# Optimization experiments

Measured on AMD Instinct MI355X. Metric: run time of the kernel, lower is better.

Reference implementation:

```python
import jax, jax.numpy as jnp
import numpy as np

D = 2  # NUM_DIM (spatial dimension)


def _mlp(x, params, activate_final=False):
    n = len(params)
    for i, (w, b) in enumerate(params):
        x = x @ w + b
        if i < n - 1 or activate_final:
            x = jnp.tanh(x)
    return x


def _glorot(key, shape):
    fan_in, fan_out = shape[0], shape[-1]
    lim = np.sqrt(6.0 / (fan_in + fan_out)).astype(np.float32)
    return jax.random.uniform(key, shape, jnp.float32, -lim, lim)


def setup_inputs() -> dict:
    key = jax.random.key(0)
    ks = iter(jax.random.split(key, 40))
    B, N, M, K, P, C = 4, 32, 64, 16, 128, 2
    AW, TW, W = 64, 256, 128
    inp = {}
    inp['phase_coords'] = jax.random.normal(next(ks), (B, N, 2 * D), jnp.float32)
    inp['boundary_coords'] = jax.random.normal(next(ks), (B, M, 2 * D), jnp.float32)
    inp['boundary'] = jax.random.uniform(next(ks), (B, M), jnp.float32)
    inp['boundary_weights'] = jax.random.uniform(next(ks), (B, M), jnp.float32)
    inp['position_coords'] = jax.random.normal(next(ks), (B, P, D), jnp.float32)
    inp['sigma'] = jax.random.uniform(next(ks), (B, P, C), jnp.float32)
    inp['velocity_coords'] = jax.random.normal(next(ks), (B, K, D), jnp.float32)
    inp['velocity_weights'] = jax.random.uniform(next(ks), (B, K), jnp.float32)
    inp['scattering_kernel'] = jax.random.uniform(next(ks), (B, N, K), jnp.float32)
    inp['self_scattering_kernel'] = jax.random.uniform(next(ks), (B, K, K), jnp.float32)
    # attention MLP: input 2*D + 2 (coords ++ local frame) -> [64, 64, 1]
    inp['aw0'] = _glorot(next(ks), (2 * D + 2, AW)); inp['ab0'] = jnp.zeros((AW,), jnp.float32)
    inp['aw1'] = _glorot(next(ks), (AW, AW)); inp['ab1'] = jnp.zeros((AW,), jnp.float32)
    inp['aw2'] = _glorot(next(ks), (AW, 1)); inp['ab2'] = jnp.zeros((1,), jnp.float32)
    # transport MLP: input 4*D + C -> [256, 256, 128], activate_final=True
    inp['tw0'] = _glorot(next(ks), (4 * D + C, TW)); inp['tb0'] = jnp.zeros((TW,), jnp.float32)
    inp['tw1'] = _glorot(next(ks), (TW, TW)); inp['tb1'] = jnp.zeros((TW,), jnp.float32)
    inp['tw2'] = _glorot(next(ks), (TW, W)); inp['tb2'] = jnp.zeros((W,), jnp.float32)
    # scattering modules: res_block_depth=2 -> one stacked layer + one final layer
    inp['sw0'] = _glorot(next(ks), (W, W))
    inp['sb0'] = jax.random.uniform(next(ks), (W,), jnp.float32, -0.1, 0.1)
    inp['sw1'] = _glorot(next(ks), (W, W))
    inp['sb1'] = jax.random.uniform(next(ks), (W,), jnp.float32, -0.1, 0.1)
    inp['out_w'] = jax.random.uniform(next(ks), (W,), jnp.float32, -0.1, 0.1)
    return inp


def _forward(phase_coords, boundary_coords, boundary, boundary_weights,
             position_coords, sigma, velocity_coords, velocity_weights,
             scattering_kernel, self_scattering_kernel,
             aw0, ab0, aw1, ab1, aw2, ab2,
             tw0, tb0, tw1, tb1, tw2, tb2,
             sw0, sb0, sw1, sb1, out_w):
    B, N, _ = phase_coords.shape
    M = boundary_coords.shape[1]
    K = velocity_coords.shape[1]
    P = position_coords.shape[1]
    C = sigma.shape[-1]
    K1 = K + 1  # phase velocity v plus the Nv quadrature velocities

    x, v = phase_coords[..., :D], phase_coords[..., D:]          # (B,N,D)
    xp, vp = boundary_coords[..., :D], boundary_coords[..., D:]  # (B,M,D)

    # all velocities at which the transport MLP is evaluated: (B,N,K1,D)
    vall = jnp.concatenate(
        [v[:, :, None, :],
         jnp.broadcast_to(velocity_coords[:, None, :, :], (B, N, K, D))], axis=2)

    # ---- CoefficientNet (geometry-masked MLP attention over coeff positions) ----
    coords = jnp.concatenate(
        [jnp.broadcast_to(x[:, :, None, :], (B, N, K1, D)), vall], axis=-1)  # (B,N,K1,2D)
    ang_g = vall / jnp.sqrt(jnp.sum(vall ** 2, axis=-1, keepdims=True) + 1e-16)
    rel = x[:, :, None, :] - position_coords[:, None, :, :]                 # (B,N,P,D)
    rel_dist = jnp.sqrt(jnp.sum(rel ** 2, axis=-1) + 1e-16)                 # (B,N,P)
    pos_local = jnp.einsum('bnpd,bnkd->bnkp', rel, ang_g)                   # (B,N,K1,P)
    ang_local = pos_local / (rel_dist[:, :, None, :] + 1e-8)
    frames = jnp.stack([ang_local, pos_local], axis=-1)                     # (B,N,K1,P,2)
    qk = jnp.concatenate(
        [jnp.broadcast_to(coords[:, :, :, None, :], (B, N, K1, P, 2 * D)), frames], axis=-1)
    logits = _mlp(qk, [(aw0, ab0), (aw1, ab1), (aw2, ab2)])[..., 0]         # (B,N,K1,P)
    attn_w = jax.nn.softmax(jnp.where(pos_local > 0, logits, -1e30), axis=-1)
    coeff = jnp.exp(-jnp.einsum('bnkp,bpc->bnkc', attn_w, sigma))           # (B,N,K1,C)

    # ---- TransportModule: MLP + exp over (B,N,M,K1) ----
    t_in = jnp.concatenate([
        jnp.broadcast_to(x[:, :, None, None, :], (B, N, M, K1, D)),
        jnp.broadcast_to(vall[:, :, None, :, :], (B, N, M, K1, D)),
        jnp.broadcast_to(xp[:, None, :, None, :], (B, N, M, K1, D)),
        jnp.broadcast_to(vp[:, None, :, None, :], (B, N, M, K1, D)),
        jnp.broadcast_to(coeff[:, :, None, :, :], (B, N, M, K1, C)),
    ], axis=-1)
    g = jnp.exp(_mlp(t_in, [(tw0, tb0), (tw1, tb1), (tw2, tb2)], activate_final=True))
    act_v = g[:, :, :, 0, :]       # (B,N,M,W)  at the phase velocity
    act_vstar = g[:, :, :, 1:, :]  # (B,N,M,K,W) at the quadrature velocities

    rw_v = (1.0 - scattering_kernel) * velocity_weights[:, None, :]        # (B,N,K)
    rw_vs = (1.0 - self_scattering_kernel) * velocity_weights[:, None, :]  # (B,K,K)

    def scat_v(act, sw, sb):
        res = jnp.einsum('bnk,bnmkw->bnmw', rw_v, act)
        return jnp.tanh(jnp.einsum('iw,bnmw->bnmi', sw, res) + sb)

    def scat_vs(act, sw, sb):
        res = jnp.einsum('bij,bnmjw->bnmiw', rw_vs, act)
        return jnp.tanh(jnp.einsum('iw,bnmkw->bnmki', sw, res) + sb)

    # layer_stack block (res_block_depth - 1 = 1 layer, shared params within the layer)
    new_v = act_v + scat_v(act_vstar, sw0, sb0)
    act_vstar = act_vstar + scat_vs(act_vstar, sw0, sb0)
    act_v = new_v
    # final scattering module (fresh params) updating act_v with res_weights_v
    green = act_v + scat_v(act_vstar, sw1, sb1)

    gdot = jnp.einsum('bnmw,w->bnm', green, out_w)
    # quadrature over boundary points
    return jnp.einsum('bnm,bm->bn', gdot, boundary * boundary_weights)


def reference(phase_coords, boundary_coords, boundary, boundary_weights,
              position_coords, sigma, velocity_coords, velocity_weights,
              scattering_kernel, self_scattering_kernel,
              aw0, ab0, aw1, ab1, aw2, ab2,
              tw0, tb0, tw1, tb1, tw2, tb2,
              sw0, sb0, sw1, sb1, out_w):
    return _forward(phase_coords, boundary_coords, boundary, boundary_weights,
                    position_coords, sigma, velocity_coords, velocity_weights,
                    scattering_kernel, self_scattering_kernel,
                    aw0, ab0, aw1, ab1, aw2, ab2,
                    tw0, tb0, tw1, tb1, tw2, tb2,
                    sw0, sb0, sw1, sb1, out_w)
```

## Files before the change

### kernel.cpp

```cpp
#include <hip/hip_runtime.h>
#include <hip/hip_bf16.h>

#define BB 4
#define NN 32
#define MM 64
#define KK 16
#define KK1 17
#define PP 128
#define CC 2

typedef unsigned short ushort_t;
typedef unsigned int uint32;
typedef __attribute__((ext_vector_type(8))) short bhalf8;
typedef __attribute__((ext_vector_type(4))) float floatx4;

#define TK  2.885390082f
#define L2E 1.44269504f

__device__ __forceinline__ float tanh_pre(float xs) {
    float e = __builtin_amdgcn_exp2f(xs);
    return fmaf(-2.0f, __builtin_amdgcn_rcpf(e + 1.0f), 1.0f);
}

__device__ __forceinline__ ushort_t f2b(float f) {
    uint32 u = __float_as_uint(f);
    return (ushort_t)((u + 0x8000u) >> 16);
}
__device__ __forceinline__ float b2f(ushort_t h) {
    return __uint_as_float(((uint32)h) << 16);
}

__device__ __forceinline__ bhalf8 tanh_uw(bhalf8 u, bhalf8 w) {
    bhalf8 h;
    #pragma unroll
    for (int j = 0; j < 8; ++j)
        h[j] = (short)f2b(tanh_pre(b2f((ushort_t)u[j]) + b2f((ushort_t)w[j])));
    return h;
}

__global__ void prep_kernel(const float* __restrict__ tw0, const float* __restrict__ tw1,
                            const float* __restrict__ tw2, const float* __restrict__ sw0,
                            const float* __restrict__ sw1, const float* __restrict__ aw0,
                            const float* __restrict__ aw1, const float* __restrict__ tb0,
                            const float* __restrict__ bcoord,
                            ushort_t* __restrict__ W1t, ushort_t* __restrict__ W2t,
                            ushort_t* __restrict__ S0t, ushort_t* __restrict__ S1t,
                            ushort_t* __restrict__ W0a, ushort_t* __restrict__ W1a,
                            ushort_t* __restrict__ w_ws) {
    int i = blockIdx.x * 256 + threadIdx.x;
    if (i < 65536) {
        int nn = i >> 8, k = i & 255;
        W1t[i] = f2b(tw1[k * 256 + nn]);
    } else if (i < 98304) {
        int j = i - 65536; int nn = j >> 8, k = j & 255;
        W2t[j] = f2b(tw2[k * 128 + nn]);
    } else if (i < 114688) {
        S0t[i - 98304] = f2b(sw0[i - 98304]);
    } else if (i < 131072) {
        S1t[i - 114688] = f2b(sw1[i - 114688]);
    } else if (i < 133120) {
        int j = i - 131072; int nn = j >> 5, k = j & 31;
        W0a[j] = (k < 6) ? f2b(aw0[k * 64 + nn]) : (ushort_t)0;
    } else if (i < 137216) {
        int j = i - 133120; int nn = j >> 6, k = j & 63;
        W1a[j] = f2b(aw1[k * 64 + nn]);
    } else if (i < 202752) {
        int j = i - 137216;
        int m = j >> 8, c = j & 255;
        float v = bcoord[m * 4 + 0] * tw0[4 * 256 + c]
                + bcoord[m * 4 + 1] * tw0[5 * 256 + c]
                + bcoord[m * 4 + 2] * tw0[6 * 256 + c]
                + bcoord[m * 4 + 3] * tw0[7 * 256 + c]
                + tb0[c];
        w_ws[j] = f2b(v * TK);
    }
}

#define AH0S 72

__global__ __launch_bounds__(128, 4) void attn_kernel(
    const float* __restrict__ phase, const float* __restrict__ posc,
    const float* __restrict__ sigma, const float* __restrict__ velc,
    const ushort_t* __restrict__ W0a, const ushort_t* __restrict__ W1a,
    const float* __restrict__ ab0, const float* __restrict__ ab1,
    const float* __restrict__ aw2, const float* __restrict__ ab2,
    const float* __restrict__ tw0, ushort_t* __restrict__ u_ws)
{
    __shared__ __align__(16) ushort_t sAH[128 * AH0S];
    __shared__ float sPL[128];
    __shared__ float sLG[128];
    __shared__ float s_red[8];

    const int tid = threadIdx.x;
    const int wave = tid >> 6;
    const int lane = tid & 63;
    const int lrow = lane & 15;
    const int lkg  = lane >> 4;

    const int blk = blockIdx.x;
    const int b = blk / (NN * KK1);
    const int rem = blk % (NN * KK1);
    const int n = rem / KK1;
    const int k = rem % KK1;

    float x0, x1, va0, va1;
    {
        const int p = tid;
        x0 = phase[(b * NN + n) * 4 + 0];
        x1 = phase[(b * NN + n) * 4 + 1];
        if (k == 0) { va0 = phase[(b * NN + n) * 4 + 2]; va1 = phase[(b * NN + n) * 4 + 3]; }
        else { va0 = velc[(b * KK + (k - 1)) * 2 + 0]; va1 = velc[(b * KK + (k - 1)) * 2 + 1]; }
        const float inv = rsqrtf(va0 * va0 + va1 * va1 + 1e-16f);
        const float ag0 = va0 * inv, ag1 = va1 * inv;
        const float px = posc[(b * PP + p) * 2 + 0];
        const float py = posc[(b * PP + p) * 2 + 1];
        const float r0 = x0 - px, r1 = x1 - py;
        const float rd = sqrtf(r0 * r0 + r1 * r1 + 1e-16f);
        const float pl = r0 * ag0 + r1 * ag1;
        const float al = pl * __builtin_amdgcn_rcpf(rd + 1e-8f);
        sPL[p] = pl;
        bhalf8 f0;
        f0[0] = (short)f2b(x0); f0[1] = (short)f2b(x1);
        f0[2] = (short)f2b(va0); f0[3] = (short)f2b(va1);
        f0[4] = (short)f2b(al); f0[5] = (short)f2b(pl);
        f0[6] = 0; f0[7] = 0;
        bhalf8 z = {0, 0, 0, 0, 0, 0, 0, 0};
        *(bhalf8*)&sAH[p * 32 + 0] = f0;
        *(bhalf8*)&sAH[p * 32 + 8] = z;
        *(bhalf8*)&sAH[p * 32 + 16] = z;
        *(bhalf8*)&sAH[p * 32 + 24] = z;
    }
    __syncthreads();

    {
        float b0v[4];
        #pragma unroll
        for (int j = 0; j < 4; ++j) b0v[j] = ab0[j * 16 + lrow] * TK;
        bhalf8 a[4];
        #pragma unroll
        for (int mtl = 0; mtl < 4; ++mtl)
            a[mtl] = *(const bhalf8*)&sAH[(wave * 64 + mtl * 16 + lrow) * 32 + lkg * 8];
        __syncthreads();
        #pragma unroll
        for (int j = 0; j < 4; ++j) {
            bhalf8 bf = *(const bhalf8*)(W0a + (j * 16 + lrow) * 32 + lkg * 8);
            #pragma unroll
            for (int mtl = 0; mtl < 4; ++mtl) {
                floatx4 c = {0.f, 0.f, 0.f, 0.f};
                c = __builtin_amdgcn_mfma_f32_16x16x32_bf16(a[mtl], bf, c, 0, 0, 0);
                #pragma unroll
                for (int q = 0; q < 4; ++q) {
                    int row = wave * 64 + mtl * 16 + lkg * 4 + q;
                    sAH[row * AH0S + j * 16 + lrow] = f2b(tanh_pre(fmaf(c[q], TK, b0v[j])));
                }
            }
        }
    }
    __syncthreads();

    {
        float b1v[4], w2v[4];
        #pragma unroll
        for (int j = 0; j < 4; ++j) { b1v[j] = ab1[j * 16 + lrow] * TK; w2v[j] = aw2[j * 16 + lrow]; }
        bhalf8 a0[4], a1[4];
        #pragma unroll
        for (int mtl = 0; mtl < 4; ++mtl) {
            int base = (wave * 64 + mtl * 16 + lrow) * AH0S;
            a0[mtl] = *(const bhalf8*)&sAH[base + lkg * 8];
            a1[mtl] = *(const bhalf8*)&sAH[base + 32 + lkg * 8];
        }
        float s[4][4];
        #pragma unroll
        for (int mtl = 0; mtl < 4; ++mtl)
            #pragma unroll
            for (int q = 0; q < 4; ++q) s[mtl][q] = 0.0f;
        #pragma unroll
        for (int j = 0; j < 4; ++j) {
            bhalf8 bf0 = *(const bhalf8*)(W1a + (j * 16 + lrow) * 64 + lkg * 8);
            bhalf8 bf1 = *(const bhalf8*)(W1a + (j * 16 + lrow) * 64 + 32 + lkg * 8);
            #pragma unroll
            for (int mtl = 0; mtl < 4; ++mtl) {
                floatx4 c = {0.f, 0.f, 0.f, 0.f};
                c = __builtin_amdgcn_mfma_f32_16x16x32_bf16(a0[mtl], bf0, c, 0, 0, 0);
                c = __builtin_amdgcn_mfma_f32_16x16x32_bf16(a1[mtl], bf1, c, 0, 0, 0);
                #pragma unroll
                for (int q = 0; q < 4; ++q)
                    s[mtl][q] += tanh_pre(fmaf(c[q], TK, b1v[j])) * w2v[j];
            }
        }
        #pragma unroll
        for (int mask = 1; mask <= 8; mask <<= 1)
            #pragma unroll
            for (int mtl = 0; mtl < 4; ++mtl)
                #pragma unroll
                for (int q = 0; q < 4; ++q)
                    s[mtl][q] += __shfl_xor(s[mtl][q], mask, 64);
        if (lrow == 0) {
            #pragma unroll
            for (int mtl = 0; mtl < 4; ++mtl)
                #pragma unroll
                for (int q = 0; q < 4; ++q)
                    sLG[wave * 64 + mtl * 16 + lkg * 4 + q] = s[mtl][q];
        }
    }
    __syncthreads();

    {
        const int p = tid;
        const float ml = (sPL[p] > 0.0f) ? (sLG[p] + ab2[0]) : -1e30f;
        const int wid = wave;
        float mv = ml;
        for (int o = 32; o > 0; o >>= 1) mv = fmaxf(mv, __shfl_xor(mv, o, 64));
        if (lane == 0) s_red[wid] = mv;
        __syncthreads();
        mv = fmaxf(s_red[0], s_red[1]);

        const float ew = __expf(ml - mv);
        float sv = ew;
        for (int o = 32; o > 0; o >>= 1) sv += __shfl_xor(sv, o, 64);
        if (lane == 0) s_red[2 + wid] = sv;
        __syncthreads();
        sv = s_red[2] + s_red[3];
        const float attn = ew * __builtin_amdgcn_rcpf(sv);

        float s0 = attn * sigma[(b * PP + p) * 2 + 0];
        float s1 = attn * sigma[(b * PP + p) * 2 + 1];
        for (int o = 32; o > 0; o >>= 1) { s0 += __shfl_xor(s0, o, 64); s1 += __shfl_xor(s1, o, 64); }
        if (lane == 0) { s_red[4 + wid] = s0; s_red[6 + wid] = s1; }
        __syncthreads();

        const float cc0 = __expf(-(s_red[4] + s_red[5]));
        const float cc1 = __expf(-(s_red[6] + s_red[7]));
        const float x0k = x0 * TK, x1k = x1 * TK;
        const float va0k = va0 * TK, va1k = va1 * TK;
        const float cc0k = cc0 * TK, cc1k = cc1 * TK;
        const int ubase = ((b * NN + n) * KK1 + k) * 256;
        for (int cc = tid; cc < 256; cc += 128) {
            float uv = x0k * tw0[cc] + x1k * tw0[256 + cc]
                     + va0k * tw0[512 + cc] + va1k * tw0[768 + cc]
                     + cc0k * tw0[2048 + cc] + cc1k * tw0[2304 + cc];
            u_ws[ubase + cc] = f2b(uv);
        }
    }
}

#define H0S  264
#define H1S  136
#define GTSs 40
#define AS2S 136

#define U_H0A  0
#define U_GTS  0
#define U_A2S  5128
#define U_H1A  8976
#define U_AS2  8976
#define U_A3   8976
#define U_AS   13600
#define F_BBW  7072
#define F_RED  7074

__global__ __launch_bounds__(256, 4) void transport_kernel(
    const float* __restrict__ boundary, const float* __restrict__ bweights,
    const float* __restrict__ vweights, const float* __restrict__ scat,
    const float* __restrict__ selfscat,
    const ushort_t* __restrict__ W1t, const ushort_t* __restrict__ W2t,
    const ushort_t* __restrict__ S0t, const ushort_t* __restrict__ S1t,
    const float* __restrict__ tb1, const float* __restrict__ tb2,
    const float* __restrict__ sb0, const float* __restrict__ sb1,
    const float* __restrict__ outw,
    const ushort_t* __restrict__ u_ws, const ushort_t* __restrict__ w_ws,
    float* __restrict__ out)
{
    __shared__ __align__(16) ushort_t smem[14160];
    float* smf = (float*)smem;

    const int tid = threadIdx.x;
    const int wave = tid >> 6;
    const int lane = tid & 63;
    const int lrow = lane & 15;
    const int lkg  = lane >> 4;

    const int blk = blockIdx.x;
    const int b  = blk >> 10;
    const int n  = (blk >> 5) & 31;
    const int mg = blk & 31;
    const int m0 = mg * 2;
    const int bn = b * NN + n;

    if (tid < 2)
        smf[F_BBW + tid] = boundary[b * MM + m0 + tid] * bweights[b * MM + m0 + tid];

    for (int idx = tid; idx < 17 * 32; idx += 256) {
        int i = idx >> 5, c = idx & 31;
        float val = 0.0f;
        if (c < 16) {
            float vw = vweights[b * KK + c];
            val = (i < 16) ? (1.0f - selfscat[(b * KK + i) * KK + c]) * vw
                           : (1.0f - scat[bn * KK + c]) * vw;
        }
        smem[U_AS + idx] = f2b(val);
    }

    {
        const int r0  = tid >> 5;
        const int oct = tid & 31;
        const int co  = oct * 8;
        const int rC  = 16 + r0;
        const int mlC = (rC >= 17) ? 1 : 0;
        const int kC  = rC - 17 * mlC;
        const bhalf8 wml0 = *(const bhalf8*)(w_ws + (b * MM + m0 + 0) * 256 + co);
        const bhalf8 wml1 = *(const bhalf8*)(w_ws + (b * MM + m0 + 1) * 256 + co);
        const bhalf8 uA = *(const bhalf8*)(u_ws + (bn * KK1 + r0) * 256 + co);
        const bhalf8 uB = *(const bhalf8*)(u_ws + (bn * KK1 + 8 + r0) * 256 + co);
        const bhalf8 uC = *(const bhalf8*)(u_ws + (bn * KK1 + kC) * 256 + co);
        const bhalf8 uD = *(const bhalf8*)(u_ws + (bn * KK1 + 7 + r0) * 256 + co);
        bhalf8 uE;
        if (r0 < 2)
            uE = *(const bhalf8*)(u_ws + (bn * KK1 + 15 + r0) * 256 + co);
        *(bhalf8*)&smem[U_H0A + r0 * H0S + co]        = tanh_uw(uA, wml0);
        *(bhalf8*)&smem[U_H0A + (8 + r0) * H0S + co]  = tanh_uw(uB, wml0);
        *(bhalf8*)&smem[U_H0A + rC * H0S + co]        = tanh_uw(uC, mlC ? wml1 : wml0);
        *(bhalf8*)&smem[U_H0A + (24 + r0) * H0S + co] = tanh_uw(uD, wml1);
        if (r0 < 2)
            *(bhalf8*)&smem[U_H0A + (32 + r0) * H0S + co] = tanh_uw(uE, wml1);
    }
    __syncthreads();

    floatx4 c2[2][3];
    #pragma unroll
    for (int j = 0; j < 2; ++j)
        #pragma unroll
        for (int mt = 0; mt < 3; ++mt) c2[j][mt] = (floatx4){0.f, 0.f, 0.f, 0.f};

    #pragma unroll
    for (int p = 0; p < 2; ++p) {
        floatx4 c1h[2][3];
        #pragma unroll
        for (int j = 0; j < 2; ++j)
            #pragma unroll
            for (int mt = 0; mt < 3; ++mt) c1h[j][mt] = (floatx4){0.f, 0.f, 0.f, 0.f};
        #pragma unroll
        for (int ksl = 0; ksl < 8; ++ksl) {
            bhalf8 a[3];
            #pragma unroll
            for (int mt = 0; mt < 3; ++mt)
                a[mt] = *(const bhalf8*)&smem[U_H0A + (mt * 16 + lrow) * H0S + ksl * 32 + lkg * 8];
            #pragma unroll
            for (int jj = 0; jj < 2; ++jj) {
                bhalf8 bf = *(const bhalf8*)(W1t + ((4 * wave + 2 * p + jj) * 16 + lrow) * 256
                                             + ksl * 32 + lkg * 8);
                #pragma unroll
                for (int mt = 0; mt < 3; ++mt)
                    c1h[jj][mt] = __builtin_amdgcn_mfma_f32_16x16x32_bf16(a[mt], bf, c1h[jj][mt], 0, 0, 0);
            }
        }
        #pragma unroll
        for (int jj = 0; jj < 2; ++jj) {
            const float bb = tb1[(4 * wave + 2 * p + jj) * 16 + lrow] * TK;
            #pragma unroll
            for (int mt = 0; mt < 3; ++mt)
                #pragma unroll
                for (int q = 0; q < 4; ++q) {
                    const int row = mt * 16 + lkg * 4 + q;
                    if (row < 34)
                        smem[U_H1A + row * H1S + wave * 32 + jj * 16 + lrow] =
                            f2b(tanh_pre(fmaf(c1h[jj][mt][q], TK, bb)));
                }
        }
        __syncthreads();
        if (p == 1) {
            bhalf8 z = {0, 0, 0, 0, 0, 0, 0, 0};
            if (tid < 128)       *(bhalf8*)&smem[U_GTS + tid * GTSs + 32] = z;
            else if (tid == 128) *(bhalf8*)&smem[U_GTS + 5120] = z;
        }
        #pragma unroll
        for (int ks = 0; ks < 4; ++ks) {
            bhalf8 a[3];
            #pragma unroll
            for (int mt = 0; mt < 3; ++mt) {
                int rr = mt * 16 + lrow;
                if (rr >= 34) rr = 32;
                a[mt] = *(const bhalf8*)&smem[U_H1A + rr * H1S + ks * 32 + lkg * 8];
            }
            #pragma unroll
            for (int j2 = 0; j2 < 2; ++j2) {
                bhalf8 bf = *(const bhalf8*)(W2t + ((2 * wave + j2) * 16 + lrow) * 256
                                             + ks * 64 + p * 32 + lkg * 8);
                #pragma unroll
                for (int mt = 0; mt < 3; ++mt)
                    c2[j2][mt] = __builtin_amdgcn_mfma_f32_16x16x32_bf16(a[mt], bf, c2[j2][mt], 0, 0, 0);
            }
        }
        if (p == 0) __syncthreads();
    }

    float gv0[2] = {0.f, 0.f}, gv1[2] = {0.f, 0.f};
    {
        #pragma unroll
        for (int j = 0; j < 2; ++j) {
            const float bb = tb2[(2 * wave + j) * 16 + lrow] * TK;
            #pragma unroll
            for (int mt = 0; mt < 3; ++mt)
                #pragma unroll
                for (int q = 0; q < 4; ++q) {
                    int row = mt * 16 + lkg * 4 + q;
                    if (row < 34) {
                        int ml = (row >= 17);
                        int k = row - ml * 17;
                        int col = (2 * wave + j) * 16 + lrow;
                        float t = tanh_pre(fmaf(c2[j][mt][q], TK, bb));
                        float g = __builtin_amdgcn_exp2f(t * L2E);
                        if (k == 0) { if (ml) gv1[j] = g; else gv0[j] = g; }
                        else        smem[U_GTS + col * GTSs + ml * 16 + (k - 1)] = f2b(g);
                    }
                }
        }
    }
    __syncthreads();

    for (int idx = tid; idx < 512; idx += 256) {
        int r = idx >> 5, c = idx & 31;
        smem[U_A2S + idx] = ((c >> 4) == r) ? smem[U_AS + 16 * 32 + (c & 15)] : (ushort_t)0;
    }
    {
        bhalf8 a0 = *(const bhalf8*)&smem[U_AS + lrow * 32 + lkg * 8];
        bhalf8 a1 = *(const bhalf8*)&smem[U_AS + 16 * 32 + lkg * 8];
        for (int m = 0; m < 2; ++m) {
            #pragma unroll
            for (int j = 0; j < 2; ++j) {
                int nt = 2 * wave + j;
                bhalf8 bf = *(const bhalf8*)&smem[U_GTS + (nt * 16 + lrow) * GTSs + m * 16 + lkg * 8];
                #pragma unroll
                for (int mt = 0; mt < 2; ++mt) {
                    floatx4 c = {0.f, 0.f, 0.f, 0.f};
                    c = __builtin_amdgcn_mfma_f32_16x16x32_bf16(mt ? a1 : a0, bf, c, 0, 0, 0);
                    #pragma unroll
                    for (int q = 0; q < 4; ++q) {
                        int ic = mt * 16 + lkg * 4 + q;
                        if (ic < 17) {
                            int r2 = (ic == 16) ? m * 17 : m * 17 + 1 + ic;
                            smem[U_AS2 + r2 * AS2S + nt * 16 + lrow] = f2b(c[q]);
                        }
                    }
                }
            }
        }
    }
    __syncthreads();

    float nv0[2] = {0.f, 0.f}, nv1[2] = {0.f, 0.f};
    {
        floatx4 c3[2][3];
        #pragma unroll
        for (int j = 0; j < 2; ++j)
            #pragma unroll
            for (int mt = 0; mt < 3; ++mt) c3[j][mt] = (floatx4){0.f, 0.f, 0.f, 0.f};
        #pragma unroll
        for (int ks = 0; ks < 4; ++ks) {
            bhalf8 a[3];
            #pragma unroll
            for (int mt = 0; mt < 3; ++mt) {
                int rr = mt * 16 + lrow;
                if (rr >= 34) rr = 32;
                a[mt] = *(const bhalf8*)&smem[U_AS2 + rr * AS2S + ks * 32 + lkg * 8];
            }
            #pragma unroll
            for (int j = 0; j < 2; ++j) {
                bhalf8 bf = *(const bhalf8*)(S0t + ((2 * wave + j) * 16 + lrow) * 128 + ks * 32 + lkg * 8);
                #pragma unroll
                for (int mt = 0; mt < 3; ++mt)
                    c3[j][mt] = __builtin_amdgcn_mfma_f32_16x16x32_bf16(a[mt], bf, c3[j][mt], 0, 0, 0);
            }
        }
        #pragma unroll
        for (int j = 0; j < 2; ++j) {
            const float bb = sb0[(2 * wave + j) * 16 + lrow] * TK;
            #pragma unroll
            for (int mt = 0; mt < 3; ++mt)
                #pragma unroll
                for (int q = 0; q < 4; ++q) {
                    int r2 = mt * 16 + lkg * 4 + q;
                    if (r2 < 34) {
                        int m = (r2 >= 17);
                        int i2 = r2 - m * 17;
                        int col = (2 * wave + j) * 16 + lrow;
                        float val = tanh_pre(fmaf(c3[j][mt][q], TK, bb));
                        if (i2 == 0) {
                            if (m) nv1[j] = gv1[j] + val; else nv0[j] = gv0[j] + val;
                        } else {
                            int cell = U_GTS + col * GTSs + m * 16 + (i2 - 1);
                            smem[cell] = f2b(b2f(smem[cell]) + val);
                        }
                    }
                }
        }
    }
    __syncthreads();

    {
        bhalf8 a = *(const bhalf8*)&smem[U_A2S + lrow * 32 + lkg * 8];
        #pragma unroll
        for (int j = 0; j < 2; ++j) {
            int nt = 2 * wave + j;
            bhalf8 bf = *(const bhalf8*)&smem[U_GTS + (nt * 16 + lrow) * GTSs + lkg * 8];
            floatx4 c = {0.f, 0.f, 0.f, 0.f};
            c = __builtin_amdgcn_mfma_f32_16x16x32_bf16(a, bf, c, 0, 0, 0);
            #pragma unroll
            for (int q = 0; q < 4; ++q) {
                int r = lkg * 4 + q;
                smem[U_A3 + r * AS2S + nt * 16 + lrow] = f2b(c[q]);
            }
        }
    }
    __syncthreads();

    float acc = 0.0f;
    {
        bhalf8 a[4];
        #pragma unroll
        for (int ks = 0; ks < 4; ++ks)
            a[ks] = *(const bhalf8*)&smem[U_A3 + lrow * AS2S + ks * 32 + lkg * 8];
        #pragma unroll
        for (int j = 0; j < 2; ++j) {
            int nt = 2 * wave + j;
            float s1v = sb1[nt * 16 + lrow] * TK;
            float owv = outw[nt * 16 + lrow];
            floatx4 c = {0.f, 0.f, 0.f, 0.f};
            #pragma unroll
            for (int ks = 0; ks < 4; ++ks) {
                bhalf8 bf = *(const bhalf8*)(S1t + (nt * 16 + lrow) * 128 + ks * 32 + lkg * 8);
                c = __builtin_amdgcn_mfma_f32_16x16x32_bf16(a[ks], bf, c, 0, 0, 0);
            }
            if (lkg == 0) {
                #pragma unroll
                for (int q = 0; q < 2; ++q) {
                    float green = (q ? nv1[j] : nv0[j]) + tanh_pre(fmaf(c[q], TK, s1v));
                    acc += green * owv * smf[F_BBW + q];
                }
            }
        }
    }
    for (int o = 32; o > 0; o >>= 1) acc += __shfl_xor(acc, o, 64);
    if (lane == 0) smf[F_RED + wave] = acc;
    __syncthreads();
    if (tid == 0) {
        float tot = smf[F_RED + 0] + smf[F_RED + 1] + smf[F_RED + 2] + smf[F_RED + 3];
        atomicAdd(&out[bn], tot);
    }
}

extern "C" void kernel_launch(void* const* d_in, const int* in_sizes, int n_in,
                              void* d_out, int out_size, void* d_ws, size_t ws_size,
                              hipStream_t stream) {
    const float* phase    = (const float*)d_in[0];
    const float* bcoord   = (const float*)d_in[1];
    const float* boundary = (const float*)d_in[2];
    const float* bweights = (const float*)d_in[3];
    const float* posc     = (const float*)d_in[4];
    const float* sigma    = (const float*)d_in[5];
    const float* velc     = (const float*)d_in[6];
    const float* vweights = (const float*)d_in[7];
    const float* scat     = (const float*)d_in[8];
    const float* selfscat = (const float*)d_in[9];
    const float* aw0 = (const float*)d_in[10];
    const float* ab0 = (const float*)d_in[11];
    const float* aw1 = (const float*)d_in[12];
    const float* ab1 = (const float*)d_in[13];
    const float* aw2 = (const float*)d_in[14];
    const float* ab2 = (const float*)d_in[15];
    const float* tw0 = (const float*)d_in[16];
    const float* tb0 = (const float*)d_in[17];
    const float* tw1 = (const float*)d_in[18];
    const float* tb1 = (const float*)d_in[19];
    const float* tw2 = (const float*)d_in[20];
    const float* tb2 = (const float*)d_in[21];
    const float* sw0 = (const float*)d_in[22];
    const float* sb0 = (const float*)d_in[23];
    const float* sw1 = (const float*)d_in[24];
    const float* sb1 = (const float*)d_in[25];
    const float* outw = (const float*)d_in[26];

    float* out = (float*)d_out;
    char* ws = (char*)d_ws;
    ushort_t* W1t  = (ushort_t*)(ws + 0);
    ushort_t* W2t  = (ushort_t*)(ws + 131072);
    ushort_t* S0t  = (ushort_t*)(ws + 196608);
    ushort_t* S1t  = (ushort_t*)(ws + 229376);
    ushort_t* W0a  = (ushort_t*)(ws + 262144);
    ushort_t* W1a  = (ushort_t*)(ws + 266240);
    ushort_t* u_ws = (ushort_t*)(ws + 274432);
    ushort_t* w_ws = (ushort_t*)(ws + 1388544);

    hipMemsetAsync(d_out, 0, (size_t)out_size * sizeof(float), stream);

    prep_kernel<<<792, 256, 0, stream>>>(tw0, tw1, tw2, sw0, sw1, aw0, aw1, tb0, bcoord,
                                         W1t, W2t, S0t, S1t, W0a, W1a, w_ws);

    attn_kernel<<<BB * NN * KK1, 128, 0, stream>>>(
        phase, posc, sigma, velc, W0a, W1a, ab0, ab1, aw2, ab2, tw0, u_ws);

    transport_kernel<<<BB * NN * 32, 256, 0, stream>>>(
        boundary, bweights, vweights, scat, selfscat,
        W1t, W2t, S0t, S1t, tb1, tb2, sb0, sb1, outw, u_ws, w_ws, out);
}
```

Measured before the change: 261.9 us.

## Widen attention kernel to 256 threads and merge softmax reductions

The attention kernel now launches 256 threads per block instead of 128, so each of the four waves handles 32 positions in the MLP MFMA stages instead of 64. The softmax sum and the sigma-weighted sums are reduced in one pass, with normalization applied afterwards, which removes one block barrier. The final projection writes one output per thread. The aim is more parallelism and less per-wave serial work in this small kernel, at the cost of more threads per block and redundant position computations in the upper half.

Result: no change. 266.0 us (+1.6%).

```diff
diff --git a/kernel.cpp b/kernel.cpp
--- a/kernel.cpp
+++ b/kernel.cpp
@@ -78,7 +78,7 @@
 
 #define AH0S 72
 
-__global__ __launch_bounds__(128, 4) void attn_kernel(
+__global__ __launch_bounds__(256, 4) void attn_kernel(
     const float* __restrict__ phase, const float* __restrict__ posc,
     const float* __restrict__ sigma, const float* __restrict__ velc,
     const ushort_t* __restrict__ W0a, const ushort_t* __restrict__ W1a,
@@ -96,6 +96,7 @@
     const int lane = tid & 63;
     const int lrow = lane & 15;
     const int lkg  = lane >> 4;
+    const int pid  = tid & 127;
 
     const int blk = blockIdx.x;
     const int b = blk / (NN * KK1);
@@ -104,12 +105,13 @@
     const int k = rem % KK1;
 
     float x0, x1, va0, va1;
-    {
-        const int p = tid;
-        x0 = phase[(b * NN + n) * 4 + 0];
-        x1 = phase[(b * NN + n) * 4 + 1];
-        if (k == 0) { va0 = phase[(b * NN + n) * 4 + 2]; va1 = phase[(b * NN + n) * 4 + 3]; }
-        else { va0 = velc[(b * KK + (k - 1)) * 2 + 0]; va1 = velc[(b * KK + (k - 1)) * 2 + 1]; }
+    x0 = phase[(b * NN + n) * 4 + 0];
+    x1 = phase[(b * NN + n) * 4 + 1];
+    if (k == 0) { va0 = phase[(b * NN + n) * 4 + 2]; va1 = phase[(b * NN + n) * 4 + 3]; }
+    else { va0 = velc[(b * KK + (k - 1)) * 2 + 0]; va1 = velc[(b * KK + (k - 1)) * 2 + 1]; }
+
+    {
+        const int p = pid;
         const float inv = rsqrtf(va0 * va0 + va1 * va1 + 1e-16f);
         const float ag0 = va0 * inv, ag1 = va1 * inv;
         const float px = posc[(b * PP + p) * 2 + 0];
@@ -118,17 +120,19 @@
         const float rd = sqrtf(r0 * r0 + r1 * r1 + 1e-16f);
         const float pl = r0 * ag0 + r1 * ag1;
         const float al = pl * __builtin_amdgcn_rcpf(rd + 1e-8f);
-        sPL[p] = pl;
-        bhalf8 f0;
-        f0[0] = (short)f2b(x0); f0[1] = (short)f2b(x1);
-        f0[2] = (short)f2b(va0); f0[3] = (short)f2b(va1);
-        f0[4] = (short)f2b(al); f0[5] = (short)f2b(pl);
-        f0[6] = 0; f0[7] = 0;
-        bhalf8 z = {0, 0, 0, 0, 0, 0, 0, 0};
-        *(bhalf8*)&sAH[p * 32 + 0] = f0;
-        *(bhalf8*)&sAH[p * 32 + 8] = z;
-        *(bhalf8*)&sAH[p * 32 + 16] = z;
-        *(bhalf8*)&sAH[p * 32 + 24] = z;
+        if (tid < 128) {
+            sPL[p] = pl;
+            bhalf8 f0;
+            f0[0] = (short)f2b(x0); f0[1] = (short)f2b(x1);
+            f0[2] = (short)f2b(va0); f0[3] = (short)f2b(va1);
+            f0[4] = (short)f2b(al); f0[5] = (short)f2b(pl);
+            f0[6] = 0; f0[7] = 0;
+            bhalf8 z = {0, 0, 0, 0, 0, 0, 0, 0};
+            *(bhalf8*)&sAH[p * 32 + 0] = f0;
+            *(bhalf8*)&sAH[p * 32 + 8] = z;
+            *(bhalf8*)&sAH[p * 32 + 16] = z;
+            *(bhalf8*)&sAH[p * 32 + 24] = z;
+        }
     }
     __syncthreads();
 
@@ -136,21 +140,21 @@
         float b0v[4];
         #pragma unroll
         for (int j = 0; j < 4; ++j) b0v[j] = ab0[j * 16 + lrow] * TK;
-        bhalf8 a[4];
-        #pragma unroll
-        for (int mtl = 0; mtl < 4; ++mtl)
-            a[mtl] = *(const bhalf8*)&sAH[(wave * 64 + mtl * 16 + lrow) * 32 + lkg * 8];
+        bhalf8 a[2];
+        #pragma unroll
+        for (int mtl = 0; mtl < 2; ++mtl)
+            a[mtl] = *(const bhalf8*)&sAH[(wave * 32 + mtl * 16 + lrow) * 32 + lkg * 8];
         __syncthreads();
         #pragma unroll
         for (int j = 0; j < 4; ++j) {
             bhalf8 bf = *(const bhalf8*)(W0a + (j * 16 + lrow) * 32 + lkg * 8);
             #pragma unroll
-            for (int mtl = 0; mtl < 4; ++mtl) {
+            for (int mtl = 0; mtl < 2; ++mtl) {
                 floatx4 c = {0.f, 0.f, 0.f, 0.f};
                 c = __builtin_amdgcn_mfma_f32_16x16x32_bf16(a[mtl], bf, c, 0, 0, 0);
                 #pragma unroll
                 for (int q = 0; q < 4; ++q) {
-                    int row = wave * 64 + mtl * 16 + lkg * 4 + q;
+                    int row = wave * 32 + mtl * 16 + lkg * 4 + q;
                     sAH[row * AH0S + j * 16 + lrow] = f2b(tanh_pre(fmaf(c[q], TK, b0v[j])));
                 }
             }
@@ -162,16 +166,16 @@
         float b1v[4], w2v[4];
         #pragma unroll
         for (int j = 0; j < 4; ++j) { b1v[j] = ab1[j * 16 + lrow] * TK; w2v[j] = aw2[j * 16 + lrow]; }
-        bhalf8 a0[4], a1[4];
-        #pragma unroll
-        for (int mtl = 0; mtl < 4; ++mtl) {
-            int base = (wave * 64 + mtl * 16 + lrow) * AH0S;
+        bhalf8 a0[2], a1[2];
+        #pragma unroll
+        for (int mtl = 0; mtl < 2; ++mtl) {
+            int base = (wave * 32 + mtl * 16 + lrow) * AH0S;
             a0[mtl] = *(const bhalf8*)&sAH[base + lkg * 8];
             a1[mtl] = *(const bhalf8*)&sAH[base + 32 + lkg * 8];
         }
-        float s[4][4];
-        #pragma unroll
-        for (int mtl = 0; mtl < 4; ++mtl)
+        float s[2][4];
+        #pragma unroll
+        for (int mtl = 0; mtl < 2; ++mtl)
             #pragma unroll
             for (int q = 0; q < 4; ++q) s[mtl][q] = 0.0f;
         #pragma unroll
@@ -179,7 +183,7 @@
             bhalf8 bf0 = *(const bhalf8*)(W1a + (j * 16 + lrow) * 64 + lkg * 8);
             bhalf8 bf1 = *(const bhalf8*)(W1a + (j * 16 + lrow) * 64 + 32 + lkg * 8);
             #pragma unroll
-            for (int mtl = 0; mtl < 4; ++mtl) {
+            for (int mtl = 0; mtl < 2; ++mtl) {
                 floatx4 c = {0.f, 0.f, 0.f, 0.f};
                 c = __builtin_amdgcn_mfma_f32_16x16x32_bf16(a0[mtl], bf0, c, 0, 0, 0);
                 c = __builtin_amdgcn_mfma_f32_16x16x32_bf16(a1[mtl], bf1, c, 0, 0, 0);
@@ -191,56 +195,53 @@
         #pragma unroll
         for (int mask = 1; mask <= 8; mask <<= 1)
             #pragma unroll
-            for (int mtl = 0; mtl < 4; ++mtl)
+            for (int mtl = 0; mtl < 2; ++mtl)
                 #pragma unroll
                 for (int q = 0; q < 4; ++q)
                     s[mtl][q] += __shfl_xor(s[mtl][q], mask, 64);
         if (lrow == 0) {
             #pragma unroll
-            for (int mtl = 0; mtl < 4; ++mtl)
+            for (int mtl = 0; mtl < 2; ++mtl)
                 #pragma unroll
                 for (int q = 0; q < 4; ++q)
-                    sLG[wave * 64 + mtl * 16 + lkg * 4 + q] = s[mtl][q];
-        }
-    }
-    __syncthreads();
-
-    {
-        const int p = tid;
+                    sLG[wave * 32 + mtl * 16 + lkg * 4 + q] = s[mtl][q];
+        }
+    }
+    __syncthreads();
+
+    {
+        const int p = pid;
         const float ml = (sPL[p] > 0.0f) ? (sLG[p] + ab2[0]) : -1e30f;
-        const int wid = wave;
         float mv = ml;
         for (int o = 32; o > 0; o >>= 1) mv = fmaxf(mv, __shfl_xor(mv, o, 64));
-        if (lane == 0) s_red[wid] = mv;
+        if (lane == 0 && wave < 2) s_red[wave] = mv;
         __syncthreads();
         mv = fmaxf(s_red[0], s_red[1]);
 
         const float ew = __expf(ml - mv);
         float sv = ew;
-        for (int o = 32; o > 0; o >>= 1) sv += __shfl_xor(sv, o, 64);
-        if (lane == 0) s_red[2 + wid] = sv;
+        float s0 = ew * sigma[(b * PP + p) * 2 + 0];
+        float s1 = ew * sigma[(b * PP + p) * 2 + 1];
+        for (int o = 32; o > 0; o >>= 1) {
+            sv += __shfl_xor(sv, o, 64);
+            s0 += __shfl_xor(s0, o, 64);
+            s1 += __shfl_xor(s1, o, 64);
+        }
+        if (lane == 0 && wave < 2) { s_red[2 + wave] = sv; s_red[4 + wave] = s0; s_red[6 + wave] = s1; }
         __syncthreads();
-        sv = s_red[2] + s_red[3];
-        const float attn = ew * __builtin_amdgcn_rcpf(sv);
-
-        float s0 = attn * sigma[(b * PP + p) * 2 + 0];
-        float s1 = attn * sigma[(b * PP + p) * 2 + 1];
-        for (int o = 32; o > 0; o >>= 1) { s0 += __shfl_xor(s0, o, 64); s1 += __shfl_xor(s1, o, 64); }
-        if (lane == 0) { s_red[4 + wid] = s0; s_red[6 + wid] = s1; }
-        __syncthreads();
-
-        const float cc0 = __expf(-(s_red[4] + s_red[5]));
-        const float cc1 = __expf(-(s_red[6] + s_red[7]));
+
+        const float rsv = __builtin_amdgcn_rcpf(s_red[2] + s_red[3]);
+        const float cc0 = __expf(-(s_red[4] + s_red[5]) * rsv);
+        const float cc1 = __expf(-(s_red[6] + s_red[7]) * rsv);
         const float x0k = x0 * TK, x1k = x1 * TK;
         const float va0k = va0 * TK, va1k = va1 * TK;
         const float cc0k = cc0 * TK, cc1k = cc1 * TK;
         const int ubase = ((b * NN + n) * KK1 + k) * 256;
-        for (int cc = tid; cc < 256; cc += 128) {
-            float uv = x0k * tw0[cc] + x1k * tw0[256 + cc]
-                     + va0k * tw0[512 + cc] + va1k * tw0[768 + cc]
-                     + cc0k * tw0[2048 + cc] + cc1k * tw0[2304 + cc];
-            u_ws[ubase + cc] = f2b(uv);
-        }
+        const int cc = tid;
+        float uv = x0k * tw0[cc] + x1k * tw0[256 + cc]
+                 + va0k * tw0[512 + cc] + va1k * tw0[768 + cc]
+                 + cc0k * tw0[2048 + cc] + cc1k * tw0[2304 + cc];
+        u_ws[ubase + cc] = f2b(uv);
     }
 }
 
@@ -596,7 +597,7 @@
     prep_kernel<<<792, 256, 0, stream>>>(tw0, tw1, tw2, sw0, sw1, aw0, aw1, tb0, bcoord,
                                          W1t, W2t, S0t, S1t, W0a, W1a, w_ws);
 
-    attn_kernel<<<BB * NN * KK1, 128, 0, stream>>>(
+    attn_kernel<<<BB * NN * KK1, 256, 0, stream>>>(
         phase, posc, sigma, velc, W0a, W1a, ab0, ab1, aw2, ab2, tw0, u_ws);
 
     transport_kernel<<<BB * NN * 32, 256, 0, stream>>>(
```
